# Performance work log

Hardware: AMD Instinct MI355X
Metric: run time of the kernel (lower is better)

## Reference

```python
import jax, jax.numpy as jnp
import numpy as np
from jax import lax

N = 4096
E = 131072
C = 128
CH = [(128, 256), (256, 512), (512, 512), (512, 256), (256, 128)]


def setup_inputs() -> dict:
    key = jax.random.key(0)
    ks = jax.random.split(key, 16)
    inp = {}
    inp["x"] = jax.random.normal(ks[0], (N, C), jnp.float32)
    src = jax.random.randint(ks[1], (E,), 0, N)
    dst = jax.random.randint(ks[2], (E,), 0, N)
    inp["edge_index"] = jnp.stack([src, dst]).astype(jnp.int32)
    for i, (ci, co) in enumerate(CH):
        inp[f"theta{i}"] = jax.random.normal(ks[3 + i], (ci, co), jnp.float32) / np.float32(np.sqrt(ci))
        inp[f"b{i}"] = jax.random.normal(ks[8 + i], (co,), jnp.float32) * 0.02
    inp["p1"] = jax.random.normal(ks[13], (256,), jnp.float32)
    inp["p2"] = jax.random.normal(ks[14], (512,), jnp.float32)
    return inp


def gcn(x, W, theta, b):
    """GCNConv with edge weights, dense-adjacency form.
    A_hat = W + I (self loops, weight 1); deg = row-sum of A_hat;
    out[i] = sum_{(r->i)} d^-1/2[r] * w * d^-1/2[i] * (x@theta)[r] + b."""
    n = W.shape[0]
    A = W + jnp.eye(n, dtype=W.dtype)
    deg = A.sum(axis=1)
    dinv = jnp.where(deg > 0, lax.rsqrt(deg), 0.0)
    An = dinv[:, None] * A * dinv[None, :]
    return An.T @ (x @ theta) + b


def augment_adj(W):
    """add_self_loops -> spspmm(A, A) -> remove_self_loops, dense form."""
    n = W.shape[0]
    A = W + jnp.eye(n, dtype=W.dtype)
    A2 = A @ A
    return A2 * (1.0 - jnp.eye(n, dtype=W.dtype))


def topk_pool(x, W, p, k):
    """TopKPooling (ratio fixed via static k, single graph)."""
    score = jnp.tanh((x @ p) / jnp.linalg.norm(p))
    vals, perm = lax.top_k(score, k)
    xp = x[perm] * vals[:, None]
    Wp = W[perm][:, perm]  # filter_adj on surviving nodes
    return xp, Wp, perm


def reference(x, edge_index, theta0, theta1, theta2, theta3, theta4,
              b0, b1, b2, b3, b4, p1, p2):
    n = x.shape[0]
    # dense weighted adjacency from edge list (edge_weight = ones, duplicates sum)
    W = jnp.zeros((n, n), x.dtype).at[edge_index[0], edge_index[1]].add(1.0)

    # down block 0
    x0 = jax.nn.relu(gcn(x, W, theta0, b0))                 # [N, 256]
    x1, W1, perm1 = topk_pool(x0, augment_adj(W), p1, n // 2)
    # down block 1
    x1b = jax.nn.relu(gcn(x1, W1, theta1, b1))              # [N/2, 512]
    x2, W2, perm2 = topk_pool(x1b, augment_adj(W1), p2, n // 4)
    # bottleneck block
    xb = jax.nn.relu(gcn(x2, W2, theta2, b2))               # [N/4, 512]
    summary = xb.mean(axis=0, keepdims=True)                # global_mean_pool, 1 graph
    # up block (i=3): edges[1]=W1, res=x1b, perm2
    up1 = jnp.zeros_like(x1b).at[perm2].set(xb)
    xu = jax.nn.relu(gcn(x1b + up1, W1, theta3, b3))        # [N/2, 256]
    # up block (i=4): edges[0]=W, res=x0, perm1
    up0 = jnp.zeros_like(x0).at[perm1].set(xu)
    xout = jax.nn.relu(gcn(x0 + up0, W, theta4, b4))        # [N, 128]
    return xout, summary
```

## Files before the change

### kernel.cpp

```cpp
#include <hip/hip_runtime.h>

#define N0 4096
#define P1K 2048
#define P2K 1024
#define SPLITS 4

typedef short bf16x8 __attribute__((ext_vector_type(8)));
typedef float f32x4 __attribute__((ext_vector_type(4)));

__device__ __forceinline__ unsigned short f2bf(float f) {
  unsigned int u = __float_as_uint(f);
  unsigned int r = (u + 0x7fff + ((u >> 16) & 1)) >> 16;
  return (unsigned short)r;
}
__device__ __forceinline__ float bf2f(unsigned short h) {
  unsigned int u = ((unsigned int)h) << 16;
  return __uint_as_float(u);
}

__device__ __forceinline__ float blockReduceSum256(float v) {
  __shared__ float sh[16];
  int lane = threadIdx.x & 63;
  int w = threadIdx.x >> 6;
#pragma unroll
  for (int o = 32; o > 0; o >>= 1) v += __shfl_down(v, o, 64);
  __syncthreads();
  if (lane == 0) sh[w] = v;
  __syncthreads();
  float r = 0.f;
  if (threadIdx.x == 0) {
    int nw = (blockDim.x + 63) >> 6;
    for (int i = 0; i < nw; ++i) r += sh[i];
  }
  return r;
}

__device__ __forceinline__ int blockScanExclusive(int v, volatile int* wsums) {
  int lane = threadIdx.x & 63, w = threadIdx.x >> 6;
  int x = v;
#pragma unroll
  for (int o = 1; o < 64; o <<= 1) {
    int y = __shfl_up(x, o, 64);
    if (lane >= o) x += y;
  }
  if (lane == 63) wsums[w] = x;
  __syncthreads();
  if (threadIdx.x < 64) {
    int nw = blockDim.x >> 6;
    int s = (threadIdx.x < nw) ? wsums[threadIdx.x] : 0;
#pragma unroll
    for (int o = 1; o < 16; o <<= 1) {
      int y = __shfl_up(s, o, 64);
      if (lane >= o) s += y;
    }
    if (threadIdx.x < nw) wsums[threadIdx.x] = s;
  }
  __syncthreads();
  int base = (w > 0) ? wsums[w - 1] : 0;
  __syncthreads();
  return base + x - v;
}

__global__ void count_edges(const int* __restrict__ src, const int* __restrict__ dst,
                            int* __restrict__ co, int* __restrict__ ci, int E) {
  int e = blockIdx.x * blockDim.x + threadIdx.x;
  if (e >= E) return;
  atomicAdd(&co[src[e]], 1);
  atomicAdd(&ci[dst[e]], 1);
}

__global__ __launch_bounds__(1024) void exscan_dual(const int* __restrict__ co,
                                                    const int* __restrict__ ci,
                                                    int* __restrict__ optr,
                                                    int* __restrict__ iptr) {
  __shared__ int ls[1024];
  const int* cnt = blockIdx.x ? ci : co;
  int* ptr = blockIdx.x ? iptr : optr;
  int t = threadIdx.x;
  int v0 = cnt[t * 4], v1 = cnt[t * 4 + 1], v2 = cnt[t * 4 + 2], v3 = cnt[t * 4 + 3];
  int s = v0 + v1 + v2 + v3;
  ls[t] = s;
  __syncthreads();
  for (int off = 1; off < 1024; off <<= 1) {
    int x = (t >= off) ? ls[t - off] : 0;
    __syncthreads();
    ls[t] += x;
    __syncthreads();
  }
  int ex = (t > 0) ? ls[t - 1] : 0;
  ptr[t * 4]     = ex;
  ptr[t * 4 + 1] = ex + v0;
  ptr[t * 4 + 2] = ex + v0 + v1;
  ptr[t * 4 + 3] = ex + v0 + v1 + v2;
  if (t == 1023) ptr[4096] = ex + s;
}

__global__ void fill_edges(const int* __restrict__ src, const int* __restrict__ dst,
                           const int* __restrict__ optr, const int* __restrict__ iptr,
                           int* __restrict__ fo, int* __restrict__ fi,
                           int* __restrict__ odst, int* __restrict__ isrc, int E) {
  int e = blockIdx.x * blockDim.x + threadIdx.x;
  if (e >= E) return;
  int s = src[e], d = dst[e];
  odst[optr[s] + atomicAdd(&fo[s], 1)] = d;
  isrc[iptr[d] + atomicAdd(&fi[d], 1)] = s;
}

__global__ void dinv0_kernel(const int* __restrict__ optr, float* __restrict__ dinv0) {
  int i = blockIdx.x * blockDim.x + threadIdx.x;
  if (i < N0) dinv0[i] = rsqrtf((float)(optr[i + 1] - optr[i]) + 1.0f);
}

__global__ void conv_T_all(const float* __restrict__ t0, const float* __restrict__ t1,
                           const float* __restrict__ t2, const float* __restrict__ t3,
                           const float* __restrict__ t4,
                           unsigned short* __restrict__ o0h, unsigned short* __restrict__ o0l,
                           unsigned short* __restrict__ o1h, unsigned short* __restrict__ o1l,
                           unsigned short* __restrict__ o2, unsigned short* __restrict__ o3,
                           unsigned short* __restrict__ o4) {
  int idx = blockIdx.x * 256 + threadIdx.x;
  if (idx < 32768) {
    int k = idx >> 8, n = idx & 255;
    float v = t0[idx];
    unsigned short h = f2bf(v);
    o0h[(size_t)n * 128 + k] = h;
    o0l[(size_t)n * 128 + k] = f2bf(v - bf2f(h));
  } else if (idx < 163840) {
    int i = idx - 32768;
    int k = i >> 9, n = i & 511;
    float v = t1[i];
    unsigned short h = f2bf(v);
    o1h[(size_t)n * 256 + k] = h;
    o1l[(size_t)n * 256 + k] = f2bf(v - bf2f(h));
  } else if (idx < 425984) {
    int i = idx - 163840;
    int k = i >> 9, n = i & 511;
    o2[(size_t)n * 512 + k] = f2bf(t2[i]);
  } else if (idx < 557056) {
    int i = idx - 425984;
    int k = i >> 8, n = i & 255;
    o3[(size_t)n * 512 + k] = f2bf(t3[i]);
  } else if (idx < 589824) {
    int i = idx - 557056;
    int k = i >> 7, n = i & 127;
    o4[(size_t)n * 256 + k] = f2bf(t4[i]);
  }
}

__global__ __launch_bounds__(256) void gemm3(const float* __restrict__ A,
                                             const unsigned short* __restrict__ BhT,
                                             const unsigned short* __restrict__ BlT,
                                             const int* __restrict__ permA,
                                             const float* __restrict__ valsA,
                                             const float* __restrict__ dinv,
                                             float* __restrict__ C,
                                             int M, int N, int K, int nbx) {
  __shared__ unsigned short Ah[64 * 64], Al[64 * 64];
  __shared__ unsigned short Bh[64 * 64], Bl[64 * 64];
  int tid = threadIdx.x;
  int by = blockIdx.x / nbx, bx = blockIdx.x % nbx;
  int row0 = by << 6, col0 = bx << 6;
  int l = tid & 63, wv = tid >> 6;
  int wr = (wv >> 1) << 5, wc = (wv & 1) << 5;
  f32x4 acc[2][2] = {};
  for (int k0 = 0; k0 < K; k0 += 64) {
#pragma unroll
    for (int it = 0; it < 2; ++it) {
      int idx = (it << 8) + tid;
      int r = idx >> 3, c8 = idx & 7;
      int sw = c8 ^ (r & 7);
      int row = row0 + r;
      int srow = permA ? permA[row] : row;
      float vs = valsA ? valsA[row] : 1.f;
      const float* Af = A + (size_t)srow * K + k0 + (c8 << 3);
      float4 f0 = *(const float4*)Af;
      float4 f1 = *(const float4*)(Af + 4);
      float vv[8] = {f0.x * vs, f0.y * vs, f0.z * vs, f0.w * vs,
                     f1.x * vs, f1.y * vs, f1.z * vs, f1.w * vs};
      uint4 uh, ul;
      unsigned short hh[8], ll[8];
#pragma unroll
      for (int q = 0; q < 8; ++q) {
        hh[q] = f2bf(vv[q]);
        ll[q] = f2bf(vv[q] - bf2f(hh[q]));
      }
      uh.x = (unsigned)hh[0] | ((unsigned)hh[1] << 16);
      uh.y = (unsigned)hh[2] | ((unsigned)hh[3] << 16);
      uh.z = (unsigned)hh[4] | ((unsigned)hh[5] << 16);
      uh.w = (unsigned)hh[6] | ((unsigned)hh[7] << 16);
      ul.x = (unsigned)ll[0] | ((unsigned)ll[1] << 16);
      ul.y = (unsigned)ll[2] | ((unsigned)ll[3] << 16);
      ul.z = (unsigned)ll[4] | ((unsigned)ll[5] << 16);
      ul.w = (unsigned)ll[6] | ((unsigned)ll[7] << 16);
      ((uint4*)Ah)[(r << 3) + sw] = uh;
      ((uint4*)Al)[(r << 3) + sw] = ul;
      ((uint4*)Bh)[(r << 3) + sw] =
          *(const uint4*)(BhT + (size_t)(col0 + r) * K + k0 + (c8 << 3));
      ((uint4*)Bl)[(r << 3) + sw] =
          *(const uint4*)(BlT + (size_t)(col0 + r) * K + k0 + (c8 << 3));
    }
    __syncthreads();
#pragma unroll
    for (int kk2 = 0; kk2 < 2; ++kk2) {
      int ch = (kk2 << 2) + (l >> 4);
      int ra = wr + (l & 15), rb = ra + 16;
      int ca = wc + (l & 15), cb = ca + 16;
      int oa0 = (ra << 6) + ((ch ^ (ra & 7)) << 3);
      int oa1 = (rb << 6) + ((ch ^ (rb & 7)) << 3);
      int ob0 = (ca << 6) + ((ch ^ (ca & 7)) << 3);
      int ob1 = (cb << 6) + ((ch ^ (cb & 7)) << 3);
      bf16x8 ah0 = *(const bf16x8*)&Ah[oa0], ah1 = *(const bf16x8*)&Ah[oa1];
      bf16x8 al0 = *(const bf16x8*)&Al[oa0], al1 = *(const bf16x8*)&Al[oa1];
      bf16x8 bh0 = *(const bf16x8*)&Bh[ob0], bh1 = *(const bf16x8*)&Bh[ob1];
      bf16x8 bl0 = *(const bf16x8*)&Bl[ob0], bl1 = *(const bf16x8*)&Bl[ob1];
      acc[0][0] = __builtin_amdgcn_mfma_f32_16x16x32_bf16(ah0, bh0, acc[0][0], 0, 0, 0);
      acc[0][1] = __builtin_amdgcn_mfma_f32_16x16x32_bf16(ah0, bh1, acc[0][1], 0, 0, 0);
      acc[1][0] = __builtin_amdgcn_mfma_f32_16x16x32_bf16(ah1, bh0, acc[1][0], 0, 0, 0);
      acc[1][1] = __builtin_amdgcn_mfma_f32_16x16x32_bf16(ah1, bh1, acc[1][1], 0, 0, 0);
      acc[0][0] = __builtin_amdgcn_mfma_f32_16x16x32_bf16(ah0, bl0, acc[0][0], 0, 0, 0);
      acc[0][1] = __builtin_amdgcn_mfma_f32_16x16x32_bf16(ah0, bl1, acc[0][1], 0, 0, 0);
      acc[1][0] = __builtin_amdgcn_mfma_f32_16x16x32_bf16(ah1, bl0, acc[1][0], 0, 0, 0);
      acc[1][1] = __builtin_amdgcn_mfma_f32_16x16x32_bf16(ah1, bl1, acc[1][1], 0, 0, 0);
      acc[0][0] = __builtin_amdgcn_mfma_f32_16x16x32_bf16(al0, bh0, acc[0][0], 0, 0, 0);
      acc[0][1] = __builtin_amdgcn_mfma_f32_16x16x32_bf16(al0, bh1, acc[0][1], 0, 0, 0);
      acc[1][0] = __builtin_amdgcn_mfma_f32_16x16x32_bf16(al1, bh0, acc[1][0], 0, 0, 0);
      acc[1][1] = __builtin_amdgcn_mfma_f32_16x16x32_bf16(al1, bh1, acc[1][1], 0, 0, 0);
    }
    __syncthreads();
  }
  int lrow = (l >> 4) << 2, lcol = l & 15;
#pragma unroll
  for (int i = 0; i < 2; ++i)
#pragma unroll
    for (int j = 0; j < 2; ++j) {
      int c = col0 + wc + (j << 4) + lcol;
      int r0 = row0 + wr + (i << 4) + lrow;
#pragma unroll
      for (int rg = 0; rg < 4; ++rg) {
        int r = r0 + rg;
        float dv = dinv ? dinv[r] : 1.f;
        C[(size_t)r * N + c] = acc[i][j][rg] * dv;
      }
    }
}

__global__ __launch_bounds__(256) void split_T(const float* __restrict__ in,
                                               unsigned short* __restrict__ oh,
                                               unsigned short* __restrict__ ol) {
  __shared__ float t[64][65];
  int by = blockIdx.x >> 3, bx = blockIdx.x & 7;
  int r0 = by << 6, c0 = bx << 6;
  for (int it = 0; it < 16; ++it) {
    int idx = (it << 8) + threadIdx.x;
    int r = idx >> 6, c = idx & 63;
    t[r][c] = in[(size_t)(r0 + r) * 512 + c0 + c];
  }
  __syncthreads();
  for (int it = 0; it < 16; ++it) {
    int idx = (it << 8) + threadIdx.x;
    int rr = idx >> 6, cc = idx & 63;
    float v = t[cc][rr];
    unsigned short h = f2bf(v);
    size_t o = (size_t)(c0 + rr) * 2048 + r0 + cc;
    oh[o] = h;
    ol[o] = f2bf(v - bf2f(h));
  }
}

template <bool ABF16>
__global__ __launch_bounds__(256) void gemm_sk(const void* __restrict__ Av,
                                               const unsigned short* __restrict__ BT,
                                               const int* __restrict__ permA,
                                               const float* __restrict__ valsA,
                                               float* __restrict__ Pf,
                                               int M, int N, int K, int nbx, int nb2d) {
  __shared__ unsigned short As[64 * 64];
  __shared__ unsigned short Bs[64 * 64];
  int tid = threadIdx.x;
  int s = blockIdx.x / nb2d;
  int r2 = blockIdx.x % nb2d;
  int by = r2 / nbx, bx = r2 % nbx;
  int row0 = by << 6, col0 = bx << 6;
  int kc = K / SPLITS;
  int ks = s * kc, ke = ks + kc;
  int l = tid & 63, wv = tid >> 6;
  int wr = (wv >> 1) << 5, wc = (wv & 1) << 5;
  f32x4 acc[2][2] = {};
  for (int k0 = ks; k0 < ke; k0 += 64) {
#pragma unroll
    for (int it = 0; it < 2; ++it) {
      int idx = (it << 8) + tid;
      int r = idx >> 3, c8 = idx & 7;
      int sw = c8 ^ (r & 7);
      if (ABF16) {
        ((uint4*)As)[(r << 3) + sw] =
            *(const uint4*)((const unsigned short*)Av + (size_t)(row0 + r) * K + k0 + (c8 << 3));
      } else {
        int row = row0 + r;
        int srow = permA ? permA[row] : row;
        float vs = valsA ? valsA[row] : 1.f;
        const float* Af = (const float*)Av + (size_t)srow * K + k0 + (c8 << 3);
        float4 f0 = *(const float4*)Af;
        float4 f1 = *(const float4*)(Af + 4);
        uint4 u;
        u.x = (unsigned)f2bf(f0.x * vs) | ((unsigned)f2bf(f0.y * vs) << 16);
        u.y = (unsigned)f2bf(f0.z * vs) | ((unsigned)f2bf(f0.w * vs) << 16);
        u.z = (unsigned)f2bf(f1.x * vs) | ((unsigned)f2bf(f1.y * vs) << 16);
        u.w = (unsigned)f2bf(f1.z * vs) | ((unsigned)f2bf(f1.w * vs) << 16);
        ((uint4*)As)[(r << 3) + sw] = u;
      }
      ((uint4*)Bs)[(r << 3) + sw] =
          *(const uint4*)(BT + (size_t)(col0 + r) * K + k0 + (c8 << 3));
    }
    __syncthreads();
#pragma unroll
    for (int kk2 = 0; kk2 < 2; ++kk2) {
      int ch = (kk2 << 2) + (l >> 4);
      int ra = wr + (l & 15), rb = ra + 16;
      int ca = wc + (l & 15), cb = ca + 16;
      bf16x8 a0 = *(const bf16x8*)&As[(ra << 6) + ((ch ^ (ra & 7)) << 3)];
      bf16x8 a1 = *(const bf16x8*)&As[(rb << 6) + ((ch ^ (rb & 7)) << 3)];
      bf16x8 b0 = *(const bf16x8*)&Bs[(ca << 6) + ((ch ^ (ca & 7)) << 3)];
      bf16x8 b1 = *(const bf16x8*)&Bs[(cb << 6) + ((ch ^ (cb & 7)) << 3)];
      acc[0][0] = __builtin_amdgcn_mfma_f32_16x16x32_bf16(a0, b0, acc[0][0], 0, 0, 0);
      acc[0][1] = __builtin_amdgcn_mfma_f32_16x16x32_bf16(a0, b1, acc[0][1], 0, 0, 0);
      acc[1][0] = __builtin_amdgcn_mfma_f32_16x16x32_bf16(a1, b0, acc[1][0], 0, 0, 0);
      acc[1][1] = __builtin_amdgcn_mfma_f32_16x16x32_bf16(a1, b1, acc[1][1], 0, 0, 0);
    }
    __syncthreads();
  }
  int lrow = (l >> 4) << 2, lcol = l & 15;
  float* P = Pf + (size_t)s * M * N;
#pragma unroll
  for (int i = 0; i < 2; ++i)
#pragma unroll
    for (int j = 0; j < 2; ++j) {
      int c = col0 + wc + (j << 4) + lcol;
      int r0 = row0 + wr + (i << 4) + lrow;
#pragma unroll
      for (int rg = 0; rg < 4; ++rg)
        P[(size_t)(r0 + rg) * N + c] = acc[i][j][rg];
    }
}

__global__ __launch_bounds__(256) void epi_red0_t(const float* __restrict__ Pf,
                                                  const float* __restrict__ dinv,
                                                  float* __restrict__ Cf,
                                                  unsigned short* __restrict__ CbT,
                                                  int M, int N, int dm) {
  __shared__ float t[64][65];
  int nbx = N >> 6;
  int by = blockIdx.x / nbx, bx = blockIdx.x % nbx;
  int r0 = by << 6, c0 = bx << 6;
  size_t MN = (size_t)M * N;
  for (int it = 0; it < 16; ++it) {
    int idx = (it << 8) + threadIdx.x;
    int r = idx >> 6, c = idx & 63;
    size_t o = (size_t)(r0 + r) * N + c0 + c;
    float v = 0.f;
#pragma unroll
    for (int s = 0; s < SPLITS; ++s) v += Pf[s * MN + o];
    float dv = 1.f;
    if (dm == 1) dv = dinv[r0 + r];
    else if (dm == 2) dv = rsqrtf(dinv[r0 + r] + 1.f);
    v *= dv;
    Cf[o] = v;
    t[r][c] = v;
  }
  __syncthreads();
  if (CbT) {
    for (int it = 0; it < 16; ++it) {
      int idx = (it << 8) + threadIdx.x;
      int rr = idx >> 6, cc = idx & 63;
      CbT[(size_t)(c0 + rr) * M + r0 + cc] = f2bf(t[cc][rr]);
    }
  }
}

__global__ __launch_bounds__(256) void epi_red1(const float* __restrict__ Pf,
                                                const float* __restrict__ Zadd,
                                                const float* __restrict__ dinv,
                                                const float* __restrict__ bias,
                                                float* __restrict__ outp, int M, int N,
                                                int dm) {
  int g = blockIdx.x * 256 + threadIdx.x;
  size_t base = (size_t)g * 4;
  size_t MN = (size_t)M * N;
  if (base >= MN) return;
  int r = (int)(base / N), c = (int)(base % N);
  float4 a = *(const float4*)&Pf[base];
#pragma unroll
  for (int s = 1; s < SPLITS; ++s) {
    float4 p = *(const float4*)&Pf[s * MN + base];
    a.x += p.x; a.y += p.y; a.z += p.z; a.w += p.w;
  }
  float4 z = *(const float4*)&Zadd[base];
  float dv = (dm == 2) ? rsqrtf(dinv[r] + 1.f) : dinv[r];
  float4 bb = *(const float4*)&bias[c];
  float4 o;
  o.x = fmaxf(dv * (a.x + z.x) + bb.x, 0.f);
  o.y = fmaxf(dv * (a.y + z.y) + bb.y, 0.f);
  o.z = fmaxf(dv * (a.z + z.z) + bb.z, 0.f);
  o.w = fmaxf(dv * (a.w + z.w) + bb.w, 0.f);
  *(float4*)&outp[base] = o;
}

__global__ __launch_bounds__(256) void epi_red1s(const float* __restrict__ Pf,
                                                 const float* __restrict__ Zadd,
                                                 const float* __restrict__ dinv,
                                                 const float* __restrict__ bias,
                                                 const float* __restrict__ pvec,
                                                 float* __restrict__ sc,
                                                 float* __restrict__ outp) {
  __shared__ float shs[2][2][2];
  int li = threadIdx.x & 127;
  int lr = threadIdx.x >> 7;
  int r = blockIdx.x * 2 + lr;
  size_t base = (size_t)r * 512 + li * 4;
  const size_t MN = (size_t)2048 * 512;
  float4 a = *(const float4*)&Pf[base];
#pragma unroll
  for (int s = 1; s < 8; ++s) {
    float4 p = *(const float4*)&Pf[s * MN + base];
    a.x += p.x; a.y += p.y; a.z += p.z; a.w += p.w;
  }
  float4 z = *(const float4*)&Zadd[base];
  float dv = dinv[r];
  float4 bb = *(const float4*)&bias[li * 4];
  float4 o;
  o.x = fmaxf(dv * (a.x + z.x) + bb.x, 0.f);
  o.y = fmaxf(dv * (a.y + z.y) + bb.y, 0.f);
  o.z = fmaxf(dv * (a.z + z.z) + bb.z, 0.f);
  o.w = fmaxf(dv * (a.w + z.w) + bb.w, 0.f);
  *(float4*)&outp[base] = o;
  float4 pv = *(const float4*)&pvec[li * 4];
  float s1 = pv.x * pv.x + pv.y * pv.y + pv.z * pv.z + pv.w * pv.w;
  float s2 = o.x * pv.x + o.y * pv.y + o.z * pv.z + o.w * pv.w;
#pragma unroll
  for (int t = 32; t > 0; t >>= 1) {
    s1 += __shfl_down(s1, t, 64);
    s2 += __shfl_down(s2, t, 64);
  }
  int wir = (threadIdx.x >> 6) & 1;
  if ((threadIdx.x & 63) == 0) { shs[lr][wir][0] = s1; shs[lr][wir][1] = s2; }
  __syncthreads();
  if ((threadIdx.x & 127) == 0) {
    float S1 = shs[lr][0][0] + shs[lr][1][0];
    float S2 = shs[lr][0][1] + shs[lr][1][1];
    sc[r] = tanhf(S2 / sqrtf(S1));
  }
}

__global__ __launch_bounds__(256) void mm_w2_mfma(const unsigned short* __restrict__ Wb,
                                                  const unsigned short* __restrict__ WbT,
                                                  const int* __restrict__ perm2,
                                                  float* __restrict__ W2f) {
  __shared__ unsigned short As[64 * 64];
  __shared__ unsigned short Bs[64 * 64];
  __shared__ int pr[64], pc[64];
  int tid = threadIdx.x;
  int s = blockIdx.x >> 8;
  int t2d = blockIdx.x & 255;
  int bx = t2d & 15, by = t2d >> 4;
  int row0 = by << 6, col0 = bx << 6;
  int ks = s * 512, ke = ks + 512;
  if (tid < 64) pr[tid] = perm2[row0 + tid];
  else if (tid < 128) pc[tid - 64] = perm2[col0 + tid - 128 + 64];
  __syncthreads();
  int l = tid & 63, wv = tid >> 6;
  int wr = (wv >> 1) << 5, wc = (wv & 1) << 5;
  f32x4 acc[2][2] = {};
  for (int k0 = ks; k0 < ke; k0 += 64) {
#pragma unroll
    for (int it = 0; it < 2; ++it) {
      int idx = (it << 8) + tid;
      int r = idx >> 3, c8 = idx & 7;
      int sw = c8 ^ (r & 7);
      ((uint4*)As)[(r << 3) + sw] =
          *(const uint4*)(Wb + (size_t)pr[r] * 2048 + k0 + (c8 << 3));
      ((uint4*)Bs)[(r << 3) + sw] =
          *(const uint4*)(WbT + (size_t)pc[r] * 2048 + k0 + (c8 << 3));
    }
    __syncthreads();
    if (tid < 64) {
      int r = tid, d = pr[r] - k0;
      if (d >= 0 && d < 64) {
        int ui = (r << 6) + (((d >> 3) ^ (r & 7)) << 3) + (d & 7);
        As[ui] = f2bf(bf2f(As[ui]) + 1.f);
      }
    } else if (tid < 128) {
      int c = tid - 64, d = pc[c] - k0;
      if (d >= 0 && d < 64) {
        int ui = (c << 6) + (((d >> 3) ^ (c & 7)) << 3) + (d & 7);
        Bs[ui] = f2bf(bf2f(Bs[ui]) + 1.f);
      }
    }
    __syncthreads();
#pragma unroll
    for (int kk2 = 0; kk2 < 2; ++kk2) {
      int ch = (kk2 << 2) + (l >> 4);
      int ra = wr + (l & 15), rb = ra + 16;
      int ca = wc + (l & 15), cb = ca + 16;
      bf16x8 a0 = *(const bf16x8*)&As[(ra << 6) + ((ch ^ (ra & 7)) << 3)];
      bf16x8 a1 = *(const bf16x8*)&As[(rb << 6) + ((ch ^ (rb & 7)) << 3)];
      bf16x8 b0 = *(const bf16x8*)&Bs[(ca << 6) + ((ch ^ (ca & 7)) << 3)];
      bf16x8 b1 = *(const bf16x8*)&Bs[(cb << 6) + ((ch ^ (cb & 7)) << 3)];
      acc[0][0] = __builtin_amdgcn_mfma_f32_16x16x32_bf16(a0, b0, acc[0][0], 0, 0, 0);
      acc[0][1] = __builtin_amdgcn_mfma_f32_16x16x32_bf16(a0, b1, acc[0][1], 0, 0, 0);
      acc[1][0] = __builtin_amdgcn_mfma_f32_16x16x32_bf16(a1, b0, acc[1][0], 0, 0, 0);
      acc[1][1] = __builtin_amdgcn_mfma_f32_16x16x32_bf16(a1, b1, acc[1][1], 0, 0, 0);
    }
    __syncthreads();
  }
  int lrow = (l >> 4) << 2, lcol = l & 15;
#pragma unroll
  for (int i = 0; i < 2; ++i)
#pragma unroll
    for (int j = 0; j < 2; ++j) {
      int c = col0 + wc + (j << 4) + lcol;
      int r0 = row0 + wr + (i << 4) + lrow;
#pragma unroll
      for (int rg = 0; rg < 4; ++rg)
        atomicAdd(&W2f[(size_t)(r0 + rg) * 1024 + c], acc[i][j][rg]);
    }
}

__global__ __launch_bounds__(256) void w2_post(const float* __restrict__ W2f,
                                               unsigned short* __restrict__ W2Tb,
                                               float* __restrict__ degsum2) {
  __shared__ float t[64][65];
  int bx = blockIdx.x & 15, by = blockIdx.x >> 4;
  int r0 = by << 6, c0 = bx << 6;
  for (int it = 0; it < 16; ++it) {
    int idx = (it << 8) + threadIdx.x;
    int r = idx >> 6, c = idx & 63;
    float v = W2f[(size_t)(r0 + r) * 1024 + c0 + c];
    if (r0 + r == c0 + c) v = 0.f;
    t[r][c] = v;
  }
  __syncthreads();
  if (threadIdx.x < 64) {
    float s = 0.f;
    for (int c = 0; c < 64; ++c) s += t[threadIdx.x][c];
    atomicAdd(&degsum2[r0 + threadIdx.x], s);
  }
  for (int it = 0; it < 16; ++it) {
    int idx = (it << 8) + threadIdx.x;
    int rr = idx >> 6, cc = idx & 63;
    W2Tb[(size_t)(c0 + rr) * 1024 + r0 + cc] = f2bf(t[cc][rr]);
  }
}

__global__ __launch_bounds__(256) void transpose_bf16(const unsigned short* __restrict__ in,
                                                      unsigned short* __restrict__ out,
                                                      int n) {
  __shared__ unsigned short t[64][65];
  int nb = n >> 6;
  int bx = blockIdx.x % nb, by = blockIdx.x / nb;
  int r0 = by << 6, c0 = bx << 6;
  for (int it = 0; it < 16; ++it) {
    int idx = (it << 8) + threadIdx.x;
    int r = idx >> 6, c = idx & 63;
    t[r][c] = in[(size_t)(r0 + r) * n + c0 + c];
  }
  __syncthreads();
  for (int it = 0; it < 16; ++it) {
    int idx = (it << 8) + threadIdx.x;
    int r = idx >> 6, c = idx & 63;
    out[(size_t)(c0 + r) * n + r0 + c] = t[c][r];
  }
}

template <int C, bool SCORE>
__global__ __launch_bounds__(256) void gcn_spmm4(const int* __restrict__ iptr,
                                                 const int* __restrict__ isrc,
                                                 const float* __restrict__ Z,
                                                 const float* __restrict__ dinv,
                                                 const float* __restrict__ bias,
                                                 const float* __restrict__ pvec,
                                                 float* __restrict__ sc,
                                                 float* __restrict__ outp) {
  constexpr int L = C / 4;
  int li = threadIdx.x % L;
  int i = blockIdx.x * (256 / L) + threadIdx.x / L;
  float4 acc = *(const float4*)(Z + (size_t)i * C + li * 4);
  int beg = iptr[i], end = iptr[i + 1];
  for (int e = beg; e < end; ++e) {
    float4 z = *(const float4*)(Z + (size_t)isrc[e] * C + li * 4);
    acc.x += z.x; acc.y += z.y; acc.z += z.z; acc.w += z.w;
  }
  float d = dinv[i];
  float4 bb = *(const float4*)(bias + li * 4);
  float4 o;
  o.x = fmaxf(d * acc.x + bb.x, 0.f);
  o.y = fmaxf(d * acc.y + bb.y, 0.f);
  o.z = fmaxf(d * acc.z + bb.z, 0.f);
  o.w = fmaxf(d * acc.w + bb.w, 0.f);
  *(float4*)(outp + (size_t)i * C + li * 4) = o;
  if (SCORE) {
    float4 pv = *(const float4*)(pvec + li * 4);
    float s1 = pv.x * pv.x + pv.y * pv.y + pv.z * pv.z + pv.w * pv.w;
    float s2 = o.x * pv.x + o.y * pv.y + o.z * pv.z + o.w * pv.w;
#pragma unroll
    for (int t = 32; t > 0; t >>= 1) {
      s1 += __shfl_down(s1, t, 64);
      s2 += __shfl_down(s2, t, 64);
    }
    if ((threadIdx.x & 63) == 0) sc[i] = tanhf(s2 / sqrtf(s1));
  }
}

__global__ void add_up(const float* base, const int* __restrict__ rank,
                       const float* __restrict__ up, float* outp, int C, int total) {
  int idx = blockIdx.x * blockDim.x + threadIdx.x;
  if (idx >= total) return;
  int r = idx / C, c = idx % C;
  int rk = rank[r];
  float v = base[idx];
  if (rk >= 0) v += up[(size_t)rk * C + c];
  outp[idx] = v;
}

__global__ __launch_bounds__(1024) void topk_select(const float* __restrict__ score,
                                                    int n, int k, int* __restrict__ perm,
                                                    float* __restrict__ vals,
                                                    int* __restrict__ rank) {
  __shared__ unsigned int keys[4096];
  __shared__ int hist[256];
  __shared__ int wsums[16];
  __shared__ unsigned int sh_prefix;
  __shared__ int sh_rem;
  int t = threadIdx.x;
  int m = n >> 10;
  for (int i = t; i < n; i += 1024) {
    unsigned int u = __float_as_uint(score[i]);
    keys[i] = u ^ ((unsigned int)((int)u >> 31) | 0x80000000u);
  }
  if (t == 0) { sh_prefix = 0u; sh_rem = k; }
  __syncthreads();
  for (int round = 0; round < 4; ++round) {
    int shift = 24 - (round << 3);
    if (t < 256) hist[t] = 0;
    __syncthreads();
    unsigned int prefix = sh_prefix;
    unsigned int maskhi = (round == 0) ? 0u : (0xFFFFFFFFu << (shift + 8));
    for (int i = t; i < n; i += 1024) {
      unsigned int kk = keys[i];
      if ((kk & maskhi) == prefix) atomicAdd(&hist[(kk >> shift) & 255], 1);
    }
    __syncthreads();
    if (t == 0) {
      int rem = sh_rem, acc = 0, b = 255;
      for (; b > 0; --b) {
        if (acc + hist[b] >= rem) break;
        acc += hist[b];
      }
      sh_rem = rem - acc;
      sh_prefix = prefix | ((unsigned int)b << shift);
    }
    __syncthreads();
  }
  unsigned int thr = sh_prefix;
  int need = sh_rem;
  int base = t * m;
  int f[4];
  int cnt = 0;
#pragma unroll
  for (int j = 0; j < 4; ++j) {
    f[j] = 0;
    if (j < m) { f[j] = (keys[base + j] == thr) ? 1 : 0; cnt += f[j]; }
  }
  int ex = blockScanExclusive(cnt, wsums);
  int sel[4];
  int scnt = 0;
#pragma unroll
  for (int j = 0; j < 4; ++j) {
    sel[j] = 0;
    if (j < m) {
      unsigned int kk = keys[base + j];
      sel[j] = (kk > thr) || (kk == thr && ex < need);
      ex += f[j];
      scnt += sel[j];
    }
  }
  int pos = blockScanExclusive(scnt, wsums);
#pragma unroll
  for (int j = 0; j < 4; ++j) {
    if (j < m) {
      int i = base + j;
      if (sel[j]) {
        unsigned int kk = keys[i];
        unsigned int u = (kk & 0x80000000u) ? (kk ^ 0x80000000u) : ~kk;
        perm[pos] = i;
        vals[pos] = __uint_as_float(u);
        rank[i] = pos;
        pos++;
      } else {
        rank[i] = -1;
      }
    }
  }
}

__global__ __launch_bounds__(256) void build_W1(const int* __restrict__ optr,
                                                const int* __restrict__ odst,
                                                const int* __restrict__ perm1,
                                                const int* __restrict__ rank1,
                                                unsigned short* __restrict__ W1b,
                                                float* __restrict__ dinv1) {
  __shared__ float row[2048];
  int a = blockIdx.x;
  int pa = perm1[a];
  for (int i = threadIdx.x; i < 2048; i += 256) row[i] = 0.f;
  __syncthreads();
  int kbeg = optr[pa], kend = optr[pa + 1];
  int nk = kend - kbeg + 1;
  int wv = threadIdx.x >> 6, lane = threadIdx.x & 63;
  for (int kidx = wv; kidx < nk; kidx += 4) {
    int k = (kidx == 0) ? pa : odst[kbeg + kidx - 1];
    int jbeg = optr[k], jend = optr[k + 1];
    for (int jj = jbeg - 1 + lane; jj < jend; jj += 64) {
      int j = (jj < jbeg) ? k : odst[jj];
      int rb = rank1[j];
      if (rb >= 0) atomicAdd(&row[rb], 1.0f);
    }
  }
  __syncthreads();
  float ssum = 0.f;
  for (int i = threadIdx.x; i < 2048; i += 256) {
    float v = (i == a) ? 0.f : row[i];
    W1b[(size_t)a * 2048 + i] = f2bf(v);
    ssum += v;
  }
  float t = blockReduceSum256(ssum);
  if (threadIdx.x == 0) dinv1[a] = rsqrtf(t + 1.0f);
}

__global__ void mean_cols(const float* __restrict__ X, int R, int C, float* __restrict__ outp) {
  int c = blockIdx.x;
  float s = 0.f;
  for (int r = threadIdx.x; r < R; r += blockDim.x) s += X[(size_t)r * C + c];
  float t = blockReduceSum256(s);
  if (threadIdx.x == 0) outp[c] = t / (float)R;
}

extern "C" void kernel_launch(void* const* d_in, const int* in_sizes, int n_in,
                              void* d_out, int out_size, void* d_ws, size_t ws_size,
                              hipStream_t stream) {
  const float* x      = (const float*)d_in[0];
  const int*   eidx   = (const int*)d_in[1];
  const float* theta0 = (const float*)d_in[2];
  const float* b0     = (const float*)d_in[3];
  const float* theta1 = (const float*)d_in[4];
  const float* b1     = (const float*)d_in[5];
  const float* theta2 = (const float*)d_in[6];
  const float* b2     = (const float*)d_in[7];
  const float* theta3 = (const float*)d_in[8];
  const float* b3     = (const float*)d_in[9];
  const float* theta4 = (const float*)d_in[10];
  const float* b4     = (const float*)d_in[11];
  const float* p1     = (const float*)d_in[12];
  const float* p2     = (const float*)d_in[13];
  const int E = in_sizes[1] / 2;
  const int* src = eidx;
  const int* dst = eidx + E;
  float* out = (float*)d_out;

  char* wsb = (char*)d_ws;
  size_t off = 0;
  auto alloc = [&](size_t bytes) -> void* {
    void* p = wsb + off;
    off = (off + bytes + 255) & ~(size_t)255;
    return p;
  };
  char* zblock = (char*)alloc((size_t)4 * N0 * 4 + P2K * 4 + (size_t)P2K * P2K * 4);
  int* cnt4 = (int*)zblock;
  float* degsum2 = (float*)(zblock + (size_t)4 * N0 * 4);
  float* W2f = (float*)(zblock + (size_t)4 * N0 * 4 + P2K * 4);
  size_t zbytes = (size_t)4 * N0 * 4 + P2K * 4 + (size_t)P2K * P2K * 4;

  int* optr  = (int*)alloc((N0 + 1) * 4);
  int* iptr  = (int*)alloc((N0 + 1) * 4);
  int* odst  = (int*)alloc((size_t)E * 4);
  int* isrc  = (int*)alloc((size_t)E * 4);
  int* perm1 = (int*)alloc(P1K * 4);
  int* rank1 = (int*)alloc(N0 * 4);
  int* perm2 = (int*)alloc(P2K * 4);
  int* rank2 = (int*)alloc(P1K * 4);
  float* dinv0 = (float*)alloc(N0 * 4);
  float* dinv1 = (float*)alloc(P1K * 4);
  float* vals1 = (float*)alloc(P1K * 4);
  float* vals2 = (float*)alloc(P2K * 4);
  float* score = (float*)alloc(N0 * 4);
  float* x0  = (float*)alloc((size_t)N0 * 256 * 4);
  float* x1b = (float*)alloc((size_t)P1K * 512 * 4);
  float* xb  = (float*)alloc((size_t)P2K * 512 * 4);
  float* xu  = (float*)alloc((size_t)P1K * 256 * 4);
  float* SA  = (float*)alloc((size_t)P1K * 512 * 4);
  float* Pf  = (float*)alloc((size_t)8 * 1048576 * 4);
  unsigned short* W1b  = (unsigned short*)alloc((size_t)P1K * P1K * 2);
  unsigned short* W1bT = (unsigned short*)alloc((size_t)P1K * P1K * 2);
  unsigned short* W2Tb = (unsigned short*)alloc((size_t)P2K * P2K * 2);
  unsigned short* SAbT = (unsigned short*)alloc((size_t)524288 * 2);
  unsigned short* ZhT  = (unsigned short*)alloc((size_t)512 * 2048 * 2);
  unsigned short* ZlT  = (unsigned short*)alloc((size_t)512 * 2048 * 2);
  unsigned short* t0hT = (unsigned short*)alloc((size_t)256 * 128 * 2);
  unsigned short* t0lT = (unsigned short*)alloc((size_t)256 * 128 * 2);
  unsigned short* t1hT = (unsigned short*)alloc((size_t)512 * 256 * 2);
  unsigned short* t1lT = (unsigned short*)alloc((size_t)512 * 256 * 2);
  unsigned short* t2T  = (unsigned short*)alloc((size_t)512 * 512 * 2);
  unsigned short* t3T  = (unsigned short*)alloc((size_t)256 * 512 * 2);
  unsigned short* t4T  = (unsigned short*)alloc((size_t)128 * 256 * 2);
  (void)ws_size; (void)n_in; (void)out_size;

  int* co = cnt4;
  int* ci = cnt4 + N0;
  int* fo = cnt4 + 2 * N0;
  int* fi = cnt4 + 3 * N0;

  hipMemsetAsync(zblock, 0, zbytes, stream);
  count_edges<<<E / 256, 256, 0, stream>>>(src, dst, co, ci, E);
  exscan_dual<<<2, 1024, 0, stream>>>(co, ci, optr, iptr);
  fill_edges<<<E / 256, 256, 0, stream>>>(src, dst, optr, iptr, fo, fi, odst, isrc, E);
  dinv0_kernel<<<N0 / 256, 256, 0, stream>>>(optr, dinv0);
  conv_T_all<<<2304, 256, 0, stream>>>(theta0, theta1, theta2, theta3, theta4,
                                       t0hT, t0lT, t1hT, t1lT, t2T, t3T, t4T);

  gemm3<<<64 * 4, 256, 0, stream>>>(x, t0hT, t0lT, nullptr, nullptr, dinv0, SA,
                                    4096, 256, 128, 4);
  gcn_spmm4<256, true><<<1024, 256, 0, stream>>>(iptr, isrc, SA, dinv0, b0, p1, score, x0);

  topk_select<<<1, 1024, 0, stream>>>(score, 4096, 2048, perm1, vals1, rank1);
  build_W1<<<2048, 256, 0, stream>>>(optr, odst, perm1, rank1, W1b, dinv1);
  transpose_bf16<<<(2048 / 64) * (2048 / 64), 256, 0, stream>>>(W1b, W1bT, 2048);

  gemm3<<<32 * 8, 256, 0, stream>>>(x0, t1hT, t1lT, perm1, vals1, dinv1, SA,
                                    2048, 512, 256, 8);
  split_T<<<256, 256, 0, stream>>>(SA, ZhT, ZlT);
  gemm_sk<true><<<128 * SPLITS, 256, 0, stream>>>(W1bT, ZhT, nullptr, nullptr, Pf,
                                                  2048, 512, 2048, 8, 128);
  gemm_sk<true><<<128 * SPLITS, 256, 0, stream>>>(W1bT, ZlT, nullptr, nullptr,
                                                  Pf + (size_t)4 * 2048 * 512,
                                                  2048, 512, 2048, 8, 128);
  epi_red1s<<<1024, 256, 0, stream>>>(Pf, SA, dinv1, b1, p2, score, x1b);

  topk_select<<<1, 1024, 0, stream>>>(score, 2048, 1024, perm2, vals2, rank2);
  mm_w2_mfma<<<256 * SPLITS, 256, 0, stream>>>(W1b, W1bT, perm2, W2f);
  w2_post<<<256, 256, 0, stream>>>(W2f, W2Tb, degsum2);

  gemm_sk<false><<<128 * SPLITS, 256, 0, stream>>>(x1b, t2T, perm2, vals2, Pf,
                                                   1024, 512, 512, 8, 128);
  epi_red0_t<<<128, 256, 0, stream>>>(Pf, degsum2, SA, SAbT, 1024, 512, 2);
  gemm_sk<true><<<128 * SPLITS, 256, 0, stream>>>(W2Tb, SAbT, nullptr, nullptr, Pf,
                                                  1024, 512, 1024, 8, 128);
  epi_red1<<<1024 * 512 / 1024, 256, 0, stream>>>(Pf, SA, degsum2, b2, xb, 1024, 512, 2);
  mean_cols<<<512, 256, 0, stream>>>(xb, 1024, 512, out + 524288);

  add_up<<<2048 * 512 / 256, 256, 0, stream>>>(x1b, rank2, xb, x1b, 512, 2048 * 512);
  gemm_sk<false><<<128 * SPLITS, 256, 0, stream>>>(x1b, t3T, nullptr, nullptr, Pf,
                                                   2048, 256, 512, 4, 128);
  epi_red0_t<<<128, 256, 0, stream>>>(Pf, dinv1, SA, SAbT, 2048, 256, 1);
  gemm_sk<true><<<128 * SPLITS, 256, 0, stream>>>(W1bT, SAbT, nullptr, nullptr, Pf,
                                                  2048, 256, 2048, 4, 128);
  epi_red1<<<2048 * 256 / 1024, 256, 0, stream>>>(Pf, SA, dinv1, b3, xu, 2048, 256, 1);

  add_up<<<4096 * 256 / 256, 256, 0, stream>>>(x0, rank1, xu, x0, 256, 4096 * 256);
  gemm_sk<false><<<128 * SPLITS, 256, 0, stream>>>(x0, t4T, nullptr, nullptr, Pf,
                                                   4096, 128, 256, 2, 128);
  epi_red0_t<<<128, 256, 0, stream>>>(Pf, dinv0, SA, nullptr, 4096, 128, 1);
  gcn_spmm4<128, false><<<512, 256, 0, stream>>>(iptr, isrc, SA, dinv0, b4, nullptr, nullptr,
                                                 out);
}
```

Baseline: 346.6 us.

## Fuse transpose-split into gemm3, dual-B split-K GEMM, and fold up-scatter into epilogues

Computes dinv0 inside the exscan kernel, which removes one launch. The gemm3 epilogue now writes the transposed bf16 hi/lo split of its output through shared memory, so the separate split_T pass is gone. The two split-K GEMMs over the hi and lo parts become one kernel that multiplies against both B tiles, so the A tile is loaded once and the partial buffer shrinks. The add_up kernels are replaced by having epi_red1 add its result into the residual at perm rows. This cuts launches and memory traffic, but the scatter is a read-modify-write that assumes perm has no duplicate indices.

Measured after the change: 331.3 us. 4.4% less time.

```diff
diff --git a/kernel.cpp b/kernel.cpp
--- a/kernel.cpp
+++ b/kernel.cpp
@@ -72,7 +72,8 @@
 __global__ __launch_bounds__(1024) void exscan_dual(const int* __restrict__ co,
                                                     const int* __restrict__ ci,
                                                     int* __restrict__ optr,
-                                                    int* __restrict__ iptr) {
+                                                    int* __restrict__ iptr,
+                                                    float* __restrict__ dinv0) {
   __shared__ int ls[1024];
   const int* cnt = blockIdx.x ? ci : co;
   int* ptr = blockIdx.x ? iptr : optr;
@@ -93,6 +94,12 @@
   ptr[t * 4 + 2] = ex + v0 + v1;
   ptr[t * 4 + 3] = ex + v0 + v1 + v2;
   if (t == 1023) ptr[4096] = ex + s;
+  if (blockIdx.x == 0) {
+    dinv0[t * 4]     = rsqrtf((float)v0 + 1.f);
+    dinv0[t * 4 + 1] = rsqrtf((float)v1 + 1.f);
+    dinv0[t * 4 + 2] = rsqrtf((float)v2 + 1.f);
+    dinv0[t * 4 + 3] = rsqrtf((float)v3 + 1.f);
+  }
 }
 
 __global__ void fill_edges(const int* __restrict__ src, const int* __restrict__ dst,
@@ -104,11 +111,6 @@
   int s = src[e], d = dst[e];
   odst[optr[s] + atomicAdd(&fo[s], 1)] = d;
   isrc[iptr[d] + atomicAdd(&fi[d], 1)] = s;
-}
-
-__global__ void dinv0_kernel(const int* __restrict__ optr, float* __restrict__ dinv0) {
-  int i = blockIdx.x * blockDim.x + threadIdx.x;
-  if (i < N0) dinv0[i] = rsqrtf((float)(optr[i + 1] - optr[i]) + 1.0f);
 }
 
 __global__ void conv_T_all(const float* __restrict__ t0, const float* __restrict__ t1,
@@ -147,6 +149,7 @@
   }
 }
 
+template <bool TOUT>
 __global__ __launch_bounds__(256) void gemm3(const float* __restrict__ A,
                                              const unsigned short* __restrict__ BhT,
                                              const unsigned short* __restrict__ BlT,
@@ -154,9 +157,14 @@
                                              const float* __restrict__ valsA,
                                              const float* __restrict__ dinv,
                                              float* __restrict__ C,
+                                             unsigned short* __restrict__ ChT,
+                                             unsigned short* __restrict__ ClT,
                                              int M, int N, int K, int nbx) {
-  __shared__ unsigned short Ah[64 * 64], Al[64 * 64];
-  __shared__ unsigned short Bh[64 * 64], Bl[64 * 64];
+  __shared__ unsigned short U[16384];
+  unsigned short* Ah = U;
+  unsigned short* Al = U + 4096;
+  unsigned short* Bh = U + 8192;
+  unsigned short* Bl = U + 12288;
   int tid = threadIdx.x;
   int by = blockIdx.x / nbx, bx = blockIdx.x % nbx;
   int row0 = by << 6, col0 = bx << 6;
@@ -229,41 +237,35 @@
     __syncthreads();
   }
   int lrow = (l >> 4) << 2, lcol = l & 15;
+  float* tf = (float*)U;
 #pragma unroll
   for (int i = 0; i < 2; ++i)
 #pragma unroll
     for (int j = 0; j < 2; ++j) {
-      int c = col0 + wc + (j << 4) + lcol;
-      int r0 = row0 + wr + (i << 4) + lrow;
+      int lc = wc + (j << 4) + lcol;
+      int lr0 = wr + (i << 4) + lrow;
+      int c = col0 + lc;
 #pragma unroll
       for (int rg = 0; rg < 4; ++rg) {
-        int r = r0 + rg;
+        int lr = lr0 + rg;
+        int r = row0 + lr;
         float dv = dinv ? dinv[r] : 1.f;
-        C[(size_t)r * N + c] = acc[i][j][rg] * dv;
+        float v = acc[i][j][rg] * dv;
+        C[(size_t)r * N + c] = v;
+        if (TOUT) tf[lr * 65 + lc] = v;
       }
     }
-}
-
-__global__ __launch_bounds__(256) void split_T(const float* __restrict__ in,
-                                               unsigned short* __restrict__ oh,
-                                               unsigned short* __restrict__ ol) {
-  __shared__ float t[64][65];
-  int by = blockIdx.x >> 3, bx = blockIdx.x & 7;
-  int r0 = by << 6, c0 = bx << 6;
-  for (int it = 0; it < 16; ++it) {
-    int idx = (it << 8) + threadIdx.x;
-    int r = idx >> 6, c = idx & 63;
-    t[r][c] = in[(size_t)(r0 + r) * 512 + c0 + c];
-  }
-  __syncthreads();
-  for (int it = 0; it < 16; ++it) {
-    int idx = (it << 8) + threadIdx.x;
-    int rr = idx >> 6, cc = idx & 63;
-    float v = t[cc][rr];
-    unsigned short h = f2bf(v);
-    size_t o = (size_t)(c0 + rr) * 2048 + r0 + cc;
-    oh[o] = h;
-    ol[o] = f2bf(v - bf2f(h));
+  if (TOUT) {
+    __syncthreads();
+    for (int it = 0; it < 16; ++it) {
+      int idx = (it << 8) + tid;
+      int rr = idx >> 6, cc = idx & 63;
+      float v = tf[cc * 65 + rr];
+      unsigned short h = f2bf(v);
+      size_t o = (size_t)(col0 + rr) * M + row0 + cc;
+      ChT[o] = h;
+      ClT[o] = f2bf(v - bf2f(h));
+    }
   }
 }
 
@@ -343,6 +345,72 @@
     }
 }
 
+__global__ __launch_bounds__(256) void gemm_skd(const unsigned short* __restrict__ A,
+                                                const unsigned short* __restrict__ BhT,
+                                                const unsigned short* __restrict__ BlT,
+                                                float* __restrict__ Pf,
+                                                int M, int N, int K, int nbx, int nb2d) {
+  __shared__ unsigned short As[4096], Bh[4096], Bl[4096];
+  int tid = threadIdx.x;
+  int s = blockIdx.x / nb2d;
+  int r2 = blockIdx.x % nb2d;
+  int by = r2 / nbx, bx = r2 % nbx;
+  int row0 = by << 6, col0 = bx << 6;
+  int kc = K / SPLITS;
+  int ks = s * kc, ke = ks + kc;
+  int l = tid & 63, wv = tid >> 6;
+  int wr = (wv >> 1) << 5, wc = (wv & 1) << 5;
+  f32x4 acc[2][2] = {};
+  for (int k0 = ks; k0 < ke; k0 += 64) {
+#pragma unroll
+    for (int it = 0; it < 2; ++it) {
+      int idx = (it << 8) + tid;
+      int r = idx >> 3, c8 = idx & 7;
+      int sw = c8 ^ (r & 7);
+      ((uint4*)As)[(r << 3) + sw] =
+          *(const uint4*)(A + (size_t)(row0 + r) * K + k0 + (c8 << 3));
+      ((uint4*)Bh)[(r << 3) + sw] =
+          *(const uint4*)(BhT + (size_t)(col0 + r) * K + k0 + (c8 << 3));
+      ((uint4*)Bl)[(r << 3) + sw] =
+          *(const uint4*)(BlT + (size_t)(col0 + r) * K + k0 + (c8 << 3));
+    }
+    __syncthreads();
+#pragma unroll
+    for (int kk2 = 0; kk2 < 2; ++kk2) {
+      int ch = (kk2 << 2) + (l >> 4);
+      int ra = wr + (l & 15), rb = ra + 16;
+      int ca = wc + (l & 15), cb = ca + 16;
+      bf16x8 a0 = *(const bf16x8*)&As[(ra << 6) + ((ch ^ (ra & 7)) << 3)];
+      bf16x8 a1 = *(const bf16x8*)&As[(rb << 6) + ((ch ^ (rb & 7)) << 3)];
+      bf16x8 bh0 = *(const bf16x8*)&Bh[(ca << 6) + ((ch ^ (ca & 7)) << 3)];
+      bf16x8 bh1 = *(const bf16x8*)&Bh[(cb << 6) + ((ch ^ (cb & 7)) << 3)];
+      bf16x8 bl0 = *(const bf16x8*)&Bl[(ca << 6) + ((ch ^ (ca & 7)) << 3)];
+      bf16x8 bl1 = *(const bf16x8*)&Bl[(cb << 6) + ((ch ^ (cb & 7)) << 3)];
+      acc[0][0] = __builtin_amdgcn_mfma_f32_16x16x32_bf16(a0, bh0, acc[0][0], 0, 0, 0);
+      acc[0][1] = __builtin_amdgcn_mfma_f32_16x16x32_bf16(a0, bh1, acc[0][1], 0, 0, 0);
+      acc[1][0] = __builtin_amdgcn_mfma_f32_16x16x32_bf16(a1, bh0, acc[1][0], 0, 0, 0);
+      acc[1][1] = __builtin_amdgcn_mfma_f32_16x16x32_bf16(a1, bh1, acc[1][1], 0, 0, 0);
+      acc[0][0] = __builtin_amdgcn_mfma_f32_16x16x32_bf16(a0, bl0, acc[0][0], 0, 0, 0);
+      acc[0][1] = __builtin_amdgcn_mfma_f32_16x16x32_bf16(a0, bl1, acc[0][1], 0, 0, 0);
+      acc[1][0] = __builtin_amdgcn_mfma_f32_16x16x32_bf16(a1, bl0, acc[1][0], 0, 0, 0);
+      acc[1][1] = __builtin_amdgcn_mfma_f32_16x16x32_bf16(a1, bl1, acc[1][1], 0, 0, 0);
+    }
+    __syncthreads();
+  }
+  int lrow = (l >> 4) << 2, lcol = l & 15;
+  float* P = Pf + (size_t)s * M * N;
+#pragma unroll
+  for (int i = 0; i < 2; ++i)
+#pragma unroll
+    for (int j = 0; j < 2; ++j) {
+      int c = col0 + wc + (j << 4) + lcol;
+      int r0 = row0 + wr + (i << 4) + lrow;
+#pragma unroll
+      for (int rg = 0; rg < 4; ++rg)
+        P[(size_t)(r0 + rg) * N + c] = acc[i][j][rg];
+    }
+}
+
 __global__ __launch_bounds__(256) void epi_red0_t(const float* __restrict__ Pf,
                                                   const float* __restrict__ dinv,
                                                   float* __restrict__ Cf,
@@ -381,6 +449,8 @@
                                                 const float* __restrict__ Zadd,
                                                 const float* __restrict__ dinv,
                                                 const float* __restrict__ bias,
+                                                const int* __restrict__ permS,
+                                                float* __restrict__ scatterDst,
                                                 float* __restrict__ outp, int M, int N,
                                                 int dm) {
   int g = blockIdx.x * 256 + threadIdx.x;
@@ -402,7 +472,13 @@
   o.y = fmaxf(dv * (a.y + z.y) + bb.y, 0.f);
   o.z = fmaxf(dv * (a.z + z.z) + bb.z, 0.f);
   o.w = fmaxf(dv * (a.w + z.w) + bb.w, 0.f);
-  *(float4*)&outp[base] = o;
+  if (outp) *(float4*)&outp[base] = o;
+  if (permS) {
+    float4* d = (float4*)&scatterDst[(size_t)permS[r] * N + c];
+    float4 cur = *d;
+    cur.x += o.x; cur.y += o.y; cur.z += o.z; cur.w += o.w;
+    *d = cur;
+  }
 }
 
 __global__ __launch_bounds__(256) void epi_red1s(const float* __restrict__ Pf,
@@ -420,7 +496,7 @@
   const size_t MN = (size_t)2048 * 512;
   float4 a = *(const float4*)&Pf[base];
 #pragma unroll
-  for (int s = 1; s < 8; ++s) {
+  for (int s = 1; s < SPLITS; ++s) {
     float4 p = *(const float4*)&Pf[s * MN + base];
     a.x += p.x; a.y += p.y; a.z += p.z; a.w += p.w;
   }
@@ -608,17 +684,6 @@
     }
     if ((threadIdx.x & 63) == 0) sc[i] = tanhf(s2 / sqrtf(s1));
   }
-}
-
-__global__ void add_up(const float* base, const int* __restrict__ rank,
-                       const float* __restrict__ up, float* outp, int C, int total) {
-  int idx = blockIdx.x * blockDim.x + threadIdx.x;
-  if (idx >= total) return;
-  int r = idx / C, c = idx % C;
-  int rk = rank[r];
-  float v = base[idx];
-  if (rk >= 0) v += up[(size_t)rk * C + c];
-  outp[idx] = v;
 }
 
 __global__ __launch_bounds__(1024) void topk_select(const float* __restrict__ score,
@@ -795,9 +860,8 @@
   float* x0  = (float*)alloc((size_t)N0 * 256 * 4);
   float* x1b = (float*)alloc((size_t)P1K * 512 * 4);
   float* xb  = (float*)alloc((size_t)P2K * 512 * 4);
-  float* xu  = (float*)alloc((size_t)P1K * 256 * 4);
   float* SA  = (float*)alloc((size_t)P1K * 512 * 4);
-  float* Pf  = (float*)alloc((size_t)8 * 1048576 * 4);
+  float* Pf  = (float*)alloc((size_t)SPLITS * 1048576 * 4);
   unsigned short* W1b  = (unsigned short*)alloc((size_t)P1K * P1K * 2);
   unsigned short* W1bT = (unsigned short*)alloc((size_t)P1K * P1K * 2);
   unsigned short* W2Tb = (unsigned short*)alloc((size_t)P2K * P2K * 2);
@@ -820,28 +884,22 @@
 
   hipMemsetAsync(zblock, 0, zbytes, stream);
   count_edges<<<E / 256, 256, 0, stream>>>(src, dst, co, ci, E);
-  exscan_dual<<<2, 1024, 0, stream>>>(co, ci, optr, iptr);
+  exscan_dual<<<2, 1024, 0, stream>>>(co, ci, optr, iptr, dinv0);
   fill_edges<<<E / 256, 256, 0, stream>>>(src, dst, optr, iptr, fo, fi, odst, isrc, E);
-  dinv0_kernel<<<N0 / 256, 256, 0, stream>>>(optr, dinv0);
   conv_T_all<<<2304, 256, 0, stream>>>(theta0, theta1, theta2, theta3, theta4,
                                        t0hT, t0lT, t1hT, t1lT, t2T, t3T, t4T);
 
-  gemm3<<<64 * 4, 256, 0, stream>>>(x, t0hT, t0lT, nullptr, nullptr, dinv0, SA,
-                                    4096, 256, 128, 4);
+  gemm3<false><<<64 * 4, 256, 0, stream>>>(x, t0hT, t0lT, nullptr, nullptr, dinv0, SA,
+                                           nullptr, nullptr, 4096, 256, 128, 4);
   gcn_spmm4<256, true><<<1024, 256, 0, stream>>>(iptr, isrc, SA, dinv0, b0, p1, score, x0);
 
   topk_select<<<1, 1024, 0, stream>>>(score, 4096, 2048, perm1, vals1, rank1);
   build_W1<<<2048, 256, 0, stream>>>(optr, odst, perm1, rank1, W1b, dinv1);
   transpose_bf16<<<(2048 / 64) * (2048 / 64), 256, 0, stream>>>(W1b, W1bT, 2048);
 
-  gemm3<<<32 * 8, 256, 0, stream>>>(x0, t1hT, t1lT, perm1, vals1, dinv1, SA,
-                                    2048, 512, 256, 8);
-  split_T<<<256, 256, 0, stream>>>(SA, ZhT, ZlT);
-  gemm_sk<true><<<128 * SPLITS, 256, 0, stream>>>(W1bT, ZhT, nullptr, nullptr, Pf,
-                                                  2048, 512, 2048, 8, 128);
-  gemm_sk<true><<<128 * SPLITS, 256, 0, stream>>>(W1bT, ZlT, nullptr, nullptr,
-                                                  Pf + (size_t)4 * 2048 * 512,
-                                                  2048, 512, 2048, 8, 128);
+  gemm3<true><<<32 * 8, 256, 0, stream>>>(x0, t1hT, t1lT, perm1, vals1, dinv1, SA,
+                                          ZhT, ZlT, 2048, 512, 256, 8);
+  gemm_skd<<<256 * SPLITS, 256, 0, stream>>>(W1bT, ZhT, ZlT, Pf, 2048, 512, 2048, 8, 256);
   epi_red1s<<<1024, 256, 0, stream>>>(Pf, SA, dinv1, b1, p2, score, x1b);
 
   topk_select<<<1, 1024, 0, stream>>>(score, 2048, 1024, perm2, vals2, rank2);
@@ -853,18 +911,18 @@
   epi_red0_t<<<128, 256, 0, stream>>>(Pf, degsum2, SA, SAbT, 1024, 512, 2);
   gemm_sk<true><<<128 * SPLITS, 256, 0, stream>>>(W2Tb, SAbT, nullptr, nullptr, Pf,
                                                   1024, 512, 1024, 8, 128);
-  epi_red1<<<1024 * 512 / 1024, 256, 0, stream>>>(Pf, SA, degsum2, b2, xb, 1024, 512, 2);
+  epi_red1<<<1024 * 512 / 1024, 256, 0, stream>>>(Pf, SA, degsum2, b2, perm2, x1b, xb,
+                                                  1024, 512, 2);
   mean_cols<<<512, 256, 0, stream>>>(xb, 1024, 512, out + 524288);
 
-  add_up<<<2048 * 512 / 256, 256, 0, stream>>>(x1b, rank2, xb, x1b, 512, 2048 * 512);
   gemm_sk<false><<<128 * SPLITS, 256, 0, stream>>>(x1b, t3T, nullptr, nullptr, Pf,
                                                    2048, 256, 512, 4, 128);
   epi_red0_t<<<128, 256, 0, stream>>>(Pf, dinv1, SA, SAbT, 2048, 256, 1);
   gemm_sk<true><<<128 * SPLITS, 256, 0, stream>>>(W1bT, SAbT, nullptr, nullptr, Pf,
                                                   2048, 256, 2048, 4, 128);
-  epi_red1<<<2048 * 256 / 1024, 256, 0, stream>>>(Pf, SA, dinv1, b3, xu, 2048, 256, 1);
-
-  add_up<<<4096 * 256 / 256, 256, 0, stream>>>(x0, rank1, xu, x0, 256, 4096 * 256);
+  epi_red1<<<2048 * 256 / 1024, 256, 0, stream>>>(Pf, SA, dinv1, b3, perm1, x0, nullptr,
+                                                  2048, 256, 1);
+
   gemm_sk<false><<<128 * SPLITS, 256, 0, stream>>>(x0, t4T, nullptr, nullptr, Pf,
                                                    4096, 128, 256, 2, 128);
   epi_red0_t<<<128, 256, 0, stream>>>(Pf, dinv0, SA, nullptr, 4096, 128, 1);
```
